# Performance work log

Measured on AMD Instinct MI355X. Metric: run time of the kernel, lower is better.

Reference implementation:

```python
import jax, jax.numpy as jnp
import numpy as np

EPS = 1e-5

def setup_inputs() -> dict:
    key = jax.random.key(0)
    k1, k2, k3 = jax.random.split(key, 3)
    B, T, D, K = 8, 4096, 256, 2048
    x = jax.random.normal(k1, (B, T, D), dtype=jnp.float32)
    embedding_sum = jax.random.normal(k2, (K, D), dtype=jnp.float32)
    cluster_usage = jax.random.uniform(k3, (K,), dtype=jnp.float32)
    return {"x": x, "embedding_sum": embedding_sum, "cluster_usage": cluster_usage}

def reference(x, embedding_sum, cluster_usage):
    # embedding = embedding_sum / clamp(cluster_usage, eps)  -> [K, D]
    emb = embedding_sum / jnp.clip(cluster_usage, EPS, None)[:, None]
    shape = x.shape
    flat = x.reshape(-1, shape[-1])  # [N, D]
    # squared Euclidean distances (argmin-equivalent to torch.cdist p=2)
    d = (
        jnp.sum(flat * flat, axis=-1, keepdims=True)
        - 2.0 * flat @ emb.T
        + jnp.sum(emb * emb, axis=-1)
    )  # [N, K]
    flat_codes = jnp.argmin(d, axis=-1)  # [N]
    codes = flat_codes.reshape(shape[:-1])  # [B, T]
    quantized = emb[codes]  # [B, T, D]
    return quantized, codes
```

## Files before the change

kernel.cpp:

```cpp
#include <hip/hip_runtime.h>


#define EPSV 1e-5f
#define DDIM 256
#define TAU  0.4f
#define BM   128
#define BCL  128
#define NCT  8
#define RPB  8
#define KSPL 4
#define NROWS 32768

typedef __attribute__((ext_vector_type(8))) _Float16 f16x8;
typedef __attribute__((ext_vector_type(4))) float f32x4;
typedef unsigned short u16;
typedef unsigned long long u64;

__device__ __forceinline__ u16 f2h(float f) {
    f = fminf(fmaxf(f, -60000.f), 60000.f);
    const _Float16 h = (_Float16)f;
    return __builtin_bit_cast(u16, h);
}
__device__ __forceinline__ u64 packdk(float d, int k) {
    unsigned u = __builtin_bit_cast(unsigned, d);
    u = (u & 0x80000000u) ? ~u : (u | 0x80000000u);
    return ((u64)u << 32) | (unsigned)k;
}

__global__ void prep_e(const float* __restrict__ esum,
                       const float* __restrict__ usage,
                       float* __restrict__ emb,
                       float* __restrict__ emb_t,
                       u16* __restrict__ eh,
                       float* __restrict__ enorm2,
                       int* __restrict__ counter,
                       int K) {
    if (blockIdx.x == 0 && threadIdx.x == 0) *counter = 0;
    const int k = blockIdx.x;
    const int d = threadIdx.x;
    const float u = fmaxf(usage[k], EPSV);
    const float e = esum[k * DDIM + d] / u;
    emb[k * DDIM + d] = e;
    emb_t[(size_t)d * K + k] = e;
    eh[k * DDIM + d] = f2h(e);

    float s = e * e;
    #pragma unroll
    for (int off = 32; off > 0; off >>= 1) s += __shfl_down(s, off, 64);
    __shared__ float ws[4];
    if ((threadIdx.x & 63) == 0) ws[threadIdx.x >> 6] = s;
    __syncthreads();
    if (threadIdx.x == 0) enorm2[k] = ws[0] + ws[1] + ws[2] + ws[3];
}

__global__ void prep_x(const float* __restrict__ x, u16* __restrict__ xh) {
    const int n = blockIdx.x * 4 + (threadIdx.x >> 6);
    const int l = threadIdx.x & 63;
    const float4 v = *(const float4*)&x[(size_t)n * DDIM + l * 4];
    ushort4 h;
    h.x = f2h(v.x); h.y = f2h(v.y); h.z = f2h(v.z); h.w = f2h(v.w);
    *(ushort4*)&xh[(size_t)n * DDIM + l * 4] = h;
}

__global__ __launch_bounds__(256, 2) void vq_mfma(
        const u16* __restrict__ xh, const u16* __restrict__ eh,
        const float* __restrict__ enorm2,
        float* __restrict__ pm1, int* __restrict__ pi1,
        float* __restrict__ pm2, int N) {
    __shared__ __align__(16) u16 Als[BM * 64];
    __shared__ __align__(16) u16 Bls[BCL * 64];

    const int tid = threadIdx.x;
    const int l   = tid & 63;
    const int w   = tid >> 6;
    const int wr  = w >> 1, wc = w & 1;
    const int rowblk = blockIdx.x >> 1;
    const int half   = blockIdx.x & 1;
    const int n0     = rowblk * BM;
    const int cbase  = half * 1024;

    float m1[4][4], m2[4][4];
    int   i1[4][4];
    #pragma unroll
    for (int a = 0; a < 4; ++a)
        #pragma unroll
        for (int b = 0; b < 4; ++b) { m1[a][b] = 3.0e38f; m2[a][b] = 3.0e38f; i1[a][b] = 0; }

    const int sgc = (l & 7) ^ ((l >> 3) & 7);

    for (int ct = 0; ct < NCT; ++ct) {
        const int c0 = cbase + ct * BCL;
        f32x4 acc[4][4];
        #pragma unroll
        for (int a = 0; a < 4; ++a)
            #pragma unroll
            for (int b = 0; b < 4; ++b) acc[a][b] = (f32x4){0.f, 0.f, 0.f, 0.f};

        for (int ch = 0; ch < 4; ++ch) {
            const int colof = ch * 64;

            __syncthreads();
            #pragma unroll
            for (int j = 0; j < 4; ++j) {
                const int r = (w * 4 + j) * 8 + (l >> 3);
                const u16* ga = xh + (size_t)(n0 + r) * DDIM + colof + sgc * 8;
                __builtin_amdgcn_global_load_lds(
                    (const __attribute__((address_space(1))) void*)ga,
                    (__attribute__((address_space(3))) void*)((char*)Als + (w * 4 + j) * 1024),
                    16, 0, 0);
            }
            #pragma unroll
            for (int j = 0; j < 4; ++j) {
                const int r = (w * 4 + j) * 8 + (l >> 3);
                const u16* gb = eh + (size_t)(c0 + r) * DDIM + colof + sgc * 8;
                __builtin_amdgcn_global_load_lds(
                    (const __attribute__((address_space(1))) void*)gb,
                    (__attribute__((address_space(3))) void*)((char*)Bls + (w * 4 + j) * 1024),
                    16, 0, 0);
            }
            __syncthreads();

            #pragma unroll
            for (int ks = 0; ks < 2; ++ks) {
                f16x8 af[4], bfr[4];
                #pragma unroll
                for (int f = 0; f < 4; ++f) {
                    const int arow = wr * 64 + f * 16 + (l & 15);
                    const int ac   = (ks * 4 + (l >> 4)) ^ (l & 7);
                    af[f] = *(const f16x8*)((const char*)Als + arow * 128 + ac * 16);
                    const int brow = wc * 64 + f * 16 + (l & 15);
                    const int bc   = (ks * 4 + (l >> 4)) ^ (l & 7);
                    bfr[f] = *(const f16x8*)((const char*)Bls + brow * 128 + bc * 16);
                }
                #pragma unroll
                for (int fm = 0; fm < 4; ++fm)
                    #pragma unroll
                    for (int fn = 0; fn < 4; ++fn)
                        acc[fm][fn] = __builtin_amdgcn_mfma_f32_16x16x32_f16(
                            af[fm], bfr[fn], acc[fm][fn], 0, 0, 0);
            }
        }

        #pragma unroll
        for (int fn = 0; fn < 4; ++fn) {
            const int k = c0 + wc * 64 + fn * 16 + (l & 15);
            const float en = enorm2[k];
            #pragma unroll
            for (int fm = 0; fm < 4; ++fm)
                #pragma unroll
                for (int i = 0; i < 4; ++i) {
                    const float s = fmaf(-2.0f, acc[fm][fn][i], en);
                    const bool lt1 = s < m1[fm][i];
                    m2[fm][i] = fminf(m2[fm][i], fmaxf(s, m1[fm][i]));
                    i1[fm][i] = lt1 ? k : i1[fm][i];
                    m1[fm][i] = fminf(m1[fm][i], s);
                }
        }
    }

    #pragma unroll
    for (int fm = 0; fm < 4; ++fm)
        #pragma unroll
        for (int i = 0; i < 4; ++i) {
            float a1 = m1[fm][i], a2 = m2[fm][i];
            int ai = i1[fm][i];
            #pragma unroll
            for (int mask = 1; mask < 16; mask <<= 1) {
                const float b1 = __shfl_xor(a1, mask, 64);
                const int   bi = __shfl_xor(ai, mask, 64);
                const float b2 = __shfl_xor(a2, mask, 64);
                if (b1 < a1 || (b1 == a1 && bi < ai)) {
                    a2 = fminf(a1, fminf(a2, b2)); a1 = b1; ai = bi;
                } else {
                    a2 = fminf(b1, fminf(a2, b2));
                }
            }
            m1[fm][i] = a1; i1[fm][i] = ai; m2[fm][i] = a2;
        }

    __syncthreads();
    float* Sm1 = (float*)Als;
    int*   Si1 = (int*)((char*)Als + 512);
    float* Sm2 = (float*)((char*)Als + 1024);
    if (wc == 0 && (l & 15) == 0) {
        #pragma unroll
        for (int fm = 0; fm < 4; ++fm)
            #pragma unroll
            for (int i = 0; i < 4; ++i) {
                const int r = wr * 64 + fm * 16 + (l >> 4) * 4 + i;
                Sm1[r] = m1[fm][i]; Si1[r] = i1[fm][i]; Sm2[r] = m2[fm][i];
            }
    }
    __syncthreads();
    if (wc == 1 && (l & 15) == 0) {
        #pragma unroll
        for (int fm = 0; fm < 4; ++fm)
            #pragma unroll
            for (int i = 0; i < 4; ++i) {
                const int r = wr * 64 + fm * 16 + (l >> 4) * 4 + i;
                const float b1 = Sm1[r], b2 = Sm2[r];
                const int   bi = Si1[r];
                float a1 = m1[fm][i], a2 = m2[fm][i];
                int   ai = i1[fm][i];
                float M1, M2; int MI;
                if (b1 < a1 || (b1 == a1 && bi < ai)) {
                    M1 = b1; MI = bi; M2 = fminf(a1, fminf(a2, b2));
                } else {
                    M1 = a1; MI = ai; M2 = fminf(b1, fminf(a2, b2));
                }
                const int n = n0 + r;
                pm1[(size_t)half * N + n] = M1;
                pi1[(size_t)half * N + n] = MI;
                pm2[(size_t)half * N + n] = M2;
            }
    }
}

__global__ void combine(const float* __restrict__ pm1, const int* __restrict__ pi1,
                        const float* __restrict__ pm2,
                        float* __restrict__ codes_f, int* __restrict__ codes_i,
                        int* __restrict__ list, int* __restrict__ counter,
                        u64* __restrict__ packed, int N) {
    const int n = blockIdx.x * 256 + threadIdx.x;
    const float a1 = pm1[n], a2 = pm2[n];
    const int   ai = pi1[n];
    const float b1 = pm1[(size_t)N + n], b2 = pm2[(size_t)N + n];
    const int   bi = pi1[(size_t)N + n];
    float M1, M2; int MI;
    if (b1 < a1 || (b1 == a1 && bi < ai)) {
        M1 = b1; MI = bi; M2 = fminf(a1, fminf(a2, b2));
    } else {
        M1 = a1; MI = ai; M2 = fminf(b1, fminf(a2, b2));
    }
    codes_i[n] = MI;
    codes_f[n] = (float)MI;
    if (M2 - M1 < TAU) {
        packed[n] = 0xFFFFFFFFFFFFFFFFull;
        const int idx = atomicAdd(counter, 1);
        list[idx] = n;
    }
}

__global__ __launch_bounds__(256) void rescue_c(
        const float* __restrict__ x, const float* __restrict__ emb_t,
        const float* __restrict__ enorm2,
        const int* __restrict__ list, const int* __restrict__ counter,
        u64* __restrict__ packed, int K) {
    __shared__ float xs[RPB][DDIM];
    const int t = threadIdx.x;
    const int l = t & 63;
    int cnt = *counter;
    cnt = cnt < 0 ? 0 : (cnt > NROWS ? NROWS : cnt);
    if (cnt == 0) return;
    const int nblk  = (cnt + RPB - 1) / RPB;
    const int items = nblk * KSPL;
    const int kc    = K / KSPL;

    for (int wi = blockIdx.x; wi < items; wi += gridDim.x) {
        const int g = wi >> 2;
        const int q = wi & 3;
        const int base = g * RPB;
        int rows[RPB];
        #pragma unroll
        for (int r = 0; r < RPB; ++r) {
            int idx = base + r;
            rows[r] = list[idx < cnt ? idx : cnt - 1];
        }
        __syncthreads();
        #pragma unroll
        for (int r = 0; r < RPB; ++r)
            xs[r][t] = x[(size_t)rows[r] * DDIM + t];
        __syncthreads();

        float acc[RPB][2];
        #pragma unroll
        for (int r = 0; r < RPB; ++r) { acc[r][0] = 0.f; acc[r][1] = 0.f; }

        const float* eb = emb_t + q * kc + 2 * t;
        #pragma unroll 4
        for (int d = 0; d < DDIM; ++d) {
            const float2 e = *(const float2*)&eb[(size_t)d * K];
            #pragma unroll
            for (int r = 0; r < RPB; ++r) {
                const float xv = xs[r][d];
                acc[r][0] = fmaf(xv, e.x, acc[r][0]);
                acc[r][1] = fmaf(xv, e.y, acc[r][1]);
            }
        }

        const int k0 = q * kc + 2 * t;
        const float en0 = enorm2[k0], en1 = enorm2[k0 + 1];
        #pragma unroll
        for (int r = 0; r < RPB; ++r) {
            const float s0 = fmaf(-2.0f, acc[r][0], en0);
            const float s1 = fmaf(-2.0f, acc[r][1], en1);
            float bd = s0; int bk = k0;
            if (s1 < bd) { bd = s1; bk = k0 + 1; }
            #pragma unroll
            for (int m = 1; m < 64; m <<= 1) {
                const float od = __shfl_xor(bd, m, 64);
                const int   ok = __shfl_xor(bk, m, 64);
                if (od < bd || (od == bd && ok < bk)) { bd = od; bk = ok; }
            }
            if (l == 0) atomicMin(&packed[rows[r]], packdk(bd, bk));
        }
    }
}

__global__ void fixup(const u64* __restrict__ packed,
                      const int* __restrict__ list, const int* __restrict__ counter,
                      float* __restrict__ codes_f, int* __restrict__ codes_i) {
    int cnt = *counter;
    cnt = cnt < 0 ? 0 : (cnt > NROWS ? NROWS : cnt);
    const int i = blockIdx.x * 256 + threadIdx.x;
    if (i < cnt) {
        const int n = list[i];
        const int k = (int)(packed[n] & 0xFFFFFFFFull);
        codes_i[n] = k;
        codes_f[n] = (float)k;
    }
}

__global__ void gather_q(const float* __restrict__ emb,
                         const int* __restrict__ codes,
                         float* __restrict__ qout) {
    const int n = blockIdx.x * 4 + (threadIdx.x >> 6);
    const int c = threadIdx.x & 63;
    const int k = codes[n];
    *(float4*)&qout[(size_t)n * DDIM + c * 4] =
        *(const float4*)&emb[(size_t)k * DDIM + c * 4];
}

extern "C" void kernel_launch(void* const* d_in, const int* in_sizes, int n_in,
                              void* d_out, int out_size, void* d_ws, size_t ws_size,
                              hipStream_t stream) {
    const float* x     = (const float*)d_in[0];
    const float* esum  = (const float*)d_in[1];
    const float* usage = (const float*)d_in[2];
    const int K = in_sizes[2];
    const int N = in_sizes[0] / DDIM;

    char* p = (char*)d_ws;
    u64*   packed  = (u64*)p;                  p += (size_t)N * 8;
    float* emb     = (float*)p;                p += (size_t)K * DDIM * 4;
    float* emb_t   = (float*)p;                p += (size_t)K * DDIM * 4;
    float* enorm2  = (float*)p;                p += (size_t)K * 4;
    float* pm1     = (float*)p;                p += (size_t)2 * N * 4;
    float* pm2     = (float*)p;                p += (size_t)2 * N * 4;
    int*   pi1     = (int*)p;                  p += (size_t)2 * N * 4;
    int*   codes_i = (int*)p;                  p += (size_t)N * 4;
    int*   list    = (int*)p;                  p += (size_t)N * 4;
    int*   counter = (int*)p;                  p += 256;
    u16*   xh      = (u16*)p;                  p += (size_t)N * DDIM * 2;
    u16*   eh      = (u16*)p;                  p += (size_t)K * DDIM * 2;

    float* qout    = (float*)d_out;
    float* codes_f = qout + (size_t)N * DDIM;

    prep_e<<<K, 256, 0, stream>>>(esum, usage, emb, emb_t, eh, enorm2, counter, K);
    prep_x<<<N / 4, 256, 0, stream>>>(x, xh);
    vq_mfma<<<(N / BM) * 2, 256, 0, stream>>>(xh, eh, enorm2, pm1, pi1, pm2, N);
    combine<<<N / 256, 256, 0, stream>>>(pm1, pi1, pm2, codes_f, codes_i,
                                         list, counter, packed, N);
    rescue_c<<<1024, 256, 0, stream>>>(x, emb_t, enorm2, list, counter, packed, K);
    fixup<<<N / 256, 256, 0, stream>>>(packed, list, counter, codes_f, codes_i);
    gather_q<<<N / 4, 256, 0, stream>>>(emb, codes_i, qout);
}
```

Before: 122.9 us.

## Split codebook search into four parts with XCD-aware block remapping

Splits the codebook dimension across four workgroups per row block instead of two, giving 1024 workgroups rather than 512 so the GPU fills better. Block indices are remapped so that consecutive logical blocks (which share the same x rows) land on the same XCD, which should improve L2 reuse. The second-min update now uses a single fmed3 instruction. The cost is twice as many partial results to write and merge in the combine kernel, and each workgroup reloads its x tile for its shorter codebook slice.

After: 128.4 us. 4.5% more time.

```diff
diff --git a/kernel.cpp b/kernel.cpp
--- a/kernel.cpp
+++ b/kernel.cpp
@@ -6,7 +6,8 @@
 #define TAU  0.4f
 #define BM   128
 #define BCL  128
-#define NCT  8
+#define NPART 4
+#define NCT  4
 #define RPB  8
 #define KSPL 4
 #define NROWS 32768
@@ -74,10 +75,15 @@
     const int l   = tid & 63;
     const int w   = tid >> 6;
     const int wr  = w >> 1, wc = w & 1;
-    const int rowblk = blockIdx.x >> 1;
-    const int half   = blockIdx.x & 1;
-    const int n0     = rowblk * BM;
-    const int cbase  = half * 1024;
+
+    const int nwg = (N / BM) * NPART;
+    const int q   = nwg >> 3;
+    const int pb  = blockIdx.x;
+    const int logical = (pb & 7) * q + (pb >> 3);
+    const int rowblk  = logical >> 2;
+    const int part    = logical & 3;
+    const int n0      = rowblk * BM;
+    const int cbase   = part * 512;
 
     float m1[4][4], m2[4][4];
     int   i1[4][4];
@@ -151,7 +157,7 @@
                 for (int i = 0; i < 4; ++i) {
                     const float s = fmaf(-2.0f, acc[fm][fn][i], en);
                     const bool lt1 = s < m1[fm][i];
-                    m2[fm][i] = fminf(m2[fm][i], fmaxf(s, m1[fm][i]));
+                    m2[fm][i] = __builtin_amdgcn_fmed3f(s, m1[fm][i], m2[fm][i]);
                     i1[fm][i] = lt1 ? k : i1[fm][i];
                     m1[fm][i] = fminf(m1[fm][i], s);
                 }
@@ -209,9 +215,9 @@
                     M1 = a1; MI = ai; M2 = fminf(b1, fminf(a2, b2));
                 }
                 const int n = n0 + r;
-                pm1[(size_t)half * N + n] = M1;
-                pi1[(size_t)half * N + n] = MI;
-                pm2[(size_t)half * N + n] = M2;
+                pm1[(size_t)part * N + n] = M1;
+                pi1[(size_t)part * N + n] = MI;
+                pm2[(size_t)part * N + n] = M2;
             }
     }
 }
@@ -222,15 +228,17 @@
                         int* __restrict__ list, int* __restrict__ counter,
                         u64* __restrict__ packed, int N) {
     const int n = blockIdx.x * 256 + threadIdx.x;
-    const float a1 = pm1[n], a2 = pm2[n];
-    const int   ai = pi1[n];
-    const float b1 = pm1[(size_t)N + n], b2 = pm2[(size_t)N + n];
-    const int   bi = pi1[(size_t)N + n];
-    float M1, M2; int MI;
-    if (b1 < a1 || (b1 == a1 && bi < ai)) {
-        M1 = b1; MI = bi; M2 = fminf(a1, fminf(a2, b2));
-    } else {
-        M1 = a1; MI = ai; M2 = fminf(b1, fminf(a2, b2));
+    float M1 = pm1[n], M2 = pm2[n];
+    int   MI = pi1[n];
+    #pragma unroll
+    for (int j = 1; j < NPART; ++j) {
+        const float b1 = pm1[(size_t)j * N + n], b2 = pm2[(size_t)j * N + n];
+        const int   bi = pi1[(size_t)j * N + n];
+        if (b1 < M1 || (b1 == M1 && bi < MI)) {
+            M2 = fminf(M1, fminf(M2, b2)); M1 = b1; MI = bi;
+        } else {
+            M2 = fminf(b1, fminf(M2, b2));
+        }
     }
     codes_i[n] = MI;
     codes_f[n] = (float)MI;
@@ -345,9 +353,9 @@
     float* emb     = (float*)p;                p += (size_t)K * DDIM * 4;
     float* emb_t   = (float*)p;                p += (size_t)K * DDIM * 4;
     float* enorm2  = (float*)p;                p += (size_t)K * 4;
-    float* pm1     = (float*)p;                p += (size_t)2 * N * 4;
-    float* pm2     = (float*)p;                p += (size_t)2 * N * 4;
-    int*   pi1     = (int*)p;                  p += (size_t)2 * N * 4;
+    float* pm1     = (float*)p;                p += (size_t)NPART * N * 4;
+    float* pm2     = (float*)p;                p += (size_t)NPART * N * 4;
+    int*   pi1     = (int*)p;                  p += (size_t)NPART * N * 4;
     int*   codes_i = (int*)p;                  p += (size_t)N * 4;
     int*   list    = (int*)p;                  p += (size_t)N * 4;
     int*   counter = (int*)p;                  p += 256;
@@ -359,7 +367,7 @@
 
     prep_e<<<K, 256, 0, stream>>>(esum, usage, emb, emb_t, eh, enorm2, counter, K);
     prep_x<<<N / 4, 256, 0, stream>>>(x, xh);
-    vq_mfma<<<(N / BM) * 2, 256, 0, stream>>>(xh, eh, enorm2, pm1, pi1, pm2, N);
+    vq_mfma<<<(N / BM) * NPART, 256, 0, stream>>>(xh, eh, enorm2, pm1, pi1, pm2, N);
     combine<<<N / 256, 256, 0, stream>>>(pm1, pi1, pm2, codes_f, codes_i,
                                          list, counter, packed, N);
     rescue_c<<<1024, 256, 0, stream>>>(x, emb_t, enorm2, list, counter, packed, K);
```
